# Optimization experiments

Measured on AMD Instinct MI355X. Metric: run time of the kernel, lower is better.

Reference implementation:

```python
import jax, jax.numpy as jnp
import numpy as np

INPUT_SIZE = 64
HIDDEN_SIZE = 256


def setup_inputs() -> dict:
    key = jax.random.key(0)
    ks = jax.random.split(key, 20)
    I, H = INPUT_SIZE, HIDDEN_SIZE
    s = 0.05
    inp = {
        "x": jax.random.normal(ks[0], (256, 512, I), jnp.float32),
        # LSTM params (PyTorch layout: [4H, in], gate order i,f,g,o)
        "w_ih": jax.random.normal(ks[1], (4 * H, I), jnp.float32) * s,
        "w_hh": jax.random.normal(ks[2], (4 * H, H), jnp.float32) * s,
        "b_ih": jax.random.normal(ks[3], (4 * H,), jnp.float32) * s,
        "b_hh": jax.random.normal(ks[4], (4 * H,), jnp.float32) * s,
        # fc_pit: H -> 64 -> 1
        "pit_w1": jax.random.normal(ks[5], (64, H), jnp.float32) * s,
        "pit_b1": jax.random.normal(ks[6], (64,), jnp.float32) * s,
        "pit_w2": jax.random.normal(ks[7], (1, 64), jnp.float32) * s,
        "pit_b2": jax.random.normal(ks[8], (1,), jnp.float32) * s,
        # fc_time: H+1 -> 64 -> 1
        "time_w1": jax.random.normal(ks[9], (64, H + 1), jnp.float32) * s,
        "time_b1": jax.random.normal(ks[10], (64,), jnp.float32) * s,
        "time_w2": jax.random.normal(ks[11], (1, 64), jnp.float32) * s,
        "time_b2": jax.random.normal(ks[12], (1,), jnp.float32) * s,
        "ar_w1": jax.random.normal(ks[13], (64, I + 2), jnp.float32) * s,
        "ar_b1": jax.random.normal(ks[14], (64,), jnp.float32) * s,
        "ar_w2": jax.random.normal(ks[15], (I, 64), jnp.float32) * s,
        "ar_b2": jax.random.normal(ks[16], (I,), jnp.float32) * s,
    }
    return inp


def _forward(x, w_ih, w_hh, b_ih, b_hh, pit_w1, pit_b1, pit_w2, pit_b2,
             time_w1, time_b1, time_w2, time_b2, ar_w1, ar_b1, ar_w2, ar_b2):
    B, S, I = x.shape
    H = w_hh.shape[1]

    def step(carry, x_orig_t):
        x_t, h, c = carry  # x_t: [B, I], h/c: [B, H]
        gates = x_t @ w_ih.T + b_ih + h @ w_hh.T + b_hh  # [B, 4H]
        i_g, f_g, g_g, o_g = jnp.split(gates, 4, axis=-1)
        i_g = jax.nn.sigmoid(i_g)
        f_g = jax.nn.sigmoid(f_g)
        g_g = jnp.tanh(g_g)
        o_g = jax.nn.sigmoid(o_g)
        c = f_g * c + i_g * g_g
        h = o_g * jnp.tanh(c)
        pit = jax.nn.relu(h @ pit_w1.T + pit_b1) @ pit_w2.T + pit_b2  # [B, 1]
        t_in = jnp.concatenate([h, pit], axis=1)  # [B, H+1]
        time = jax.nn.relu(t_in @ time_w1.T + time_b1) @ time_w2.T + time_b2  # [B, 1]
        ar_in = jnp.concatenate([pit, time, x_orig_t], axis=-1)  # [B, I+2]
        nxt = jax.nn.relu(ar_in @ ar_w1.T + ar_b1) @ ar_w2.T + ar_b2  # [B, I]
        return (nxt, h, c), (pit[:, 0], time[:, 0], nxt)

    h0 = jnp.zeros((B, H), x.dtype)
    c0 = jnp.zeros((B, H), x.dtype)
    x0 = x[:, 0, :]
    x_sbI = jnp.swapaxes(x, 0, 1)  # [S, B, I] original inputs fed at each step
    _, (pits, times, nxts) = jax.lax.scan(step, (x0, h0, c0), x_sbI)
    pit_pred = pits.T  # [B, S]
    time_pred = times.T  # [B, S]
    ar_out = jnp.concatenate([x[:, :1, :], jnp.swapaxes(nxts, 0, 1)[:, : S - 1, :]], axis=1)
    return pit_pred, time_pred, ar_out


def reference(x, w_ih, w_hh, b_ih, b_hh, pit_w1, pit_b1, pit_w2, pit_b2,
              time_w1, time_b1, time_w2, time_b2, ar_w1, ar_b1, ar_w2, ar_b2):
    return _forward(x, w_ih, w_hh, b_ih, b_hh, pit_w1, pit_b1, pit_w2, pit_b2,
                    time_w1, time_b1, time_w2, time_b2, ar_w1, ar_b1, ar_w2, ar_b2)
```

## Files before the change

### kernel.cpp

```cpp
#include <hip/hip_runtime.h>
#include <hip/hip_bf16.h>
#include <hip/hip_fp8.h>


typedef float f32x4 __attribute__((ext_vector_type(4)));
typedef short s16x8 __attribute__((ext_vector_type(8)));

#define S_LEN 512
#define I_DIM 64
#define NT    512

#define WSTRIDE8 45056
#define WSB_BF   360448
#define PREP_N   368640

#define OUT_PIT  0
#define OUT_TIME 131072
#define OUT_AR   262144

#define AF8 336
#define XLD 72

__device__ __forceinline__ float sigf(float x) {
  return 1.0f / (1.0f + __expf(-x));
}
__device__ __forceinline__ float tanh_fast(float x) {
  float c = fminf(fmaxf(x, -15.0f), 15.0f);
  float e = __expf(2.0f * c);
  return (e - 1.0f) / (e + 1.0f);
}
__device__ __forceinline__ unsigned short f2bf(float f) {
  __hip_bfloat16 h = __float2bfloat16(f);
  return *reinterpret_cast<unsigned short*>(&h);
}
__device__ __forceinline__ unsigned char f2f8(float v) {
  __hip_fp8_e4m3 q(v);
  return *reinterpret_cast<unsigned char*>(&q);
}
__device__ __forceinline__ void sync_lds() {
  asm volatile("s_waitcnt lgkmcnt(0)" ::: "memory");
  __builtin_amdgcn_s_barrier();
  asm volatile("" ::: "memory");
}
__device__ __forceinline__ void gld16(const void* g, void* l) {
  __builtin_amdgcn_global_load_lds(
      (const __attribute__((address_space(1))) unsigned int*)g,
      (__attribute__((address_space(3))) unsigned int*)l, 16, 0, 0);
}

__global__ void prep_kernel(const float* __restrict__ w_ih,
                            const float* __restrict__ w_hh,
                            const float* __restrict__ pit_w1,
                            const float* __restrict__ time_w1,
                            const float* __restrict__ ar_w1,
                            const float* __restrict__ ar_w2,
                            unsigned char* __restrict__ ws8) {
  int idx = blockIdx.x * 256 + threadIdx.x;
  if (idx >= PREP_N) return;
  if (idx < WSB_BF) {
    int w  = idx / WSTRIDE8;
    int p8 = idx - w * WSTRIDE8;
    int f  = p8 >> 9;
    int b  = p8 & 511;
    int lane = b >> 3, e = b & 7;
    int lrow = lane & 15, lgrp = lane >> 4;
    float v;
    if (f < 8) {
      int row = (w & 3) * 16 + lrow;
      int col = f * 32 + lgrp * 8 + e;
      v = (w < 4) ? pit_w1[row * 256 + col] : time_w1[row * 257 + col];
    } else {
      int g = f - 8;
      int ktidx = g >> 3, qm = g & 7;
      int kt = (ktidx < 8) ? ktidx + 2 : ktidx - 8;
      int row = (qm >> 1) * 256 + w * 32 + (qm & 1) * 16 + lrow;
      int col = kt * 32 + lgrp * 8 + e;
      v = (col < I_DIM) ? w_ih[row * I_DIM + col] : w_hh[row * 256 + col - I_DIM];
    }
    ws8[idx] = f2f8(v);
  } else {
    int e2 = idx - WSB_BF;
    int lane = (e2 >> 3) & 63;
    int e    = e2 & 7;
    int lrow = lane & 15, lgrp = lane >> 4;
    float v;
    if (e2 < 4096) {
      int f = e2 >> 9, wv = f >> 1, kt = f & 1;
      v = ar_w1[(wv * 16 + lrow) * 66 + 2 + kt * 32 + lgrp * 8 + e];
    } else {
      int f = (e2 - 4096) >> 9, wv = f >> 1, kt = f & 1;
      v = ar_w2[(wv * 16 + lrow) * 64 + kt * 32 + lgrp * 8 + e];
    }
    ((unsigned short*)(ws8 + WSB_BF))[e2] = f2bf(v);
  }
}

#define A8FRAG(kt) (*(const long*)&A_f8[lrow][(kt) * 32 + 8 * lgrp])

#define DMA4F(byteoff, slot)                                                   \
  do {                                                                         \
    const unsigned char* g_ = wg8l + (byteoff);                                \
    gld16(g_,        &stg8[wave][slot][0]);                                    \
    gld16(g_ + 1024, &stg8[wave][slot][1024]);                                 \
    gld16(g_ + 2048, &stg8[wave][slot][2048]);                                 \
    gld16(g_ + 3072, &stg8[wave][slot][3072]);                                 \
  } while (0)
#define DMA2F(byteoff, slot)                                                   \
  do {                                                                         \
    const unsigned char* g_ = wg8l + (byteoff);                                \
    gld16(g_,        &stg8[wave][slot][0]);                                    \
    gld16(g_ + 1024, &stg8[wave][slot][1024]);                                 \
  } while (0)

#define CHEADF(slot, N)                                                        \
  do {                                                                         \
    asm volatile("s_waitcnt vmcnt(" #N ")" ::: "memory");                      \
    _Pragma("unroll")                                                          \
    for (int k_ = 0; k_ < 8; ++k_) {                                           \
      long b_ = *(const long*)&stg8[wave][slot][k_ * 512 + lane * 8];          \
      hacc = __builtin_amdgcn_mfma_f32_16x16x32_fp8_fp8(hfr8[k_], b_,          \
                                                        hacc, 0, 0, 0);        \
    }                                                                          \
    asm volatile("s_waitcnt lgkmcnt(0)" ::: "memory");                         \
  } while (0)
#define GCHUNK8(af, slot, N)                                                   \
  do {                                                                         \
    asm volatile("s_waitcnt vmcnt(" #N ")" ::: "memory");                      \
    _Pragma("unroll")                                                          \
    for (int s_ = 0; s_ < 8; ++s_) {                                           \
      long b_ = *(const long*)&stg8[wave][slot][s_ * 512 + lane * 8];          \
      acc2[s_] = __builtin_amdgcn_mfma_f32_16x16x32_fp8_fp8(                   \
          (af), b_, acc2[s_], 0, 0, 0);                                        \
    }                                                                          \
    asm volatile("s_waitcnt lgkmcnt(0)" ::: "memory");                         \
  } while (0)
#define GHALF4(af, slot, N, qb)                                                \
  do {                                                                         \
    asm volatile("s_waitcnt vmcnt(" #N ")" ::: "memory");                      \
    _Pragma("unroll")                                                          \
    for (int s_ = 0; s_ < 4; ++s_) {                                           \
      long b_ = *(const long*)&stg8[wave][slot][s_ * 512 + lane * 8];          \
      acc2[(qb) + s_] = __builtin_amdgcn_mfma_f32_16x16x32_fp8_fp8(            \
          (af), b_, acc2[(qb) + s_], 0, 0, 0);                                 \
    }                                                                          \
    asm volatile("s_waitcnt lgkmcnt(0)" ::: "memory");                         \
  } while (0)

__global__ __launch_bounds__(NT, 2) void rnn_kernel(
    const float* __restrict__ x,
    const float* __restrict__ b_ih, const float* __restrict__ b_hh,
    const float* __restrict__ pit_b1, const float* __restrict__ pit_w2,
    const float* __restrict__ pit_b2,
    const float* __restrict__ time_w1, const float* __restrict__ time_b1,
    const float* __restrict__ time_w2, const float* __restrict__ time_b2,
    const float* __restrict__ ar_w1, const float* __restrict__ ar_b1,
    const float* __restrict__ ar_b2,
    const unsigned char* __restrict__ ws8,
    float* __restrict__ out)
{
  __shared__ __align__(16) unsigned char  A_f8[16][AF8];
  __shared__ __align__(16) unsigned short xo_lds[16][XLD];
  __shared__ __align__(16) unsigned short ar1_lds[16][XLD];
  __shared__ __align__(16) unsigned char  stg8[8][3][4096];
  __shared__ float pitp[4][16];
  __shared__ float timep[4][16];

  const int tid  = threadIdx.x;
  const int wave = tid >> 6;
  const int lane = tid & 63;
  const int lrow = lane & 15;
  const int lgrp = lane >> 4;
  const int b0   = blockIdx.x * 16;
  const int hcol = (wave & 3) * 16 + lrow;
  const unsigned char* wg8l = ws8 + wave * WSTRIDE8 + lane * 16;
  const unsigned char* wg8  = ws8 + wave * WSTRIDE8;
  const unsigned short* wsb = (const unsigned short*)(ws8 + WSB_BF);

  for (int i = tid; i < 16 * AF8; i += NT) (&A_f8[0][0])[i] = 0;

  float gbias[8];
#pragma unroll
  for (int qm = 0; qm < 8; ++qm) {
    int g = (qm >> 1) * 256 + wave * 32 + (qm & 1) * 16 + lrow;
    gbias[qm] = b_ih[g] + b_hh[g];
  }
  s16x8 arw[2];
  float pb1v = 0, pw2v = 0, tb1v = 0, tw2v = 0, twlv = 0;
  float ab1v = 0, arpv = 0, artv = 0, ab2v = 0;
  if (wave < 4) {
    arw[0] = *(const s16x8*)&wsb[((wave & 3) * 2 + 0) * 512 + lane * 8];
    arw[1] = *(const s16x8*)&wsb[((wave & 3) * 2 + 1) * 512 + lane * 8];
    pb1v = pit_b1[hcol]; pw2v = pit_w2[hcol];
    ab1v = ar_b1[hcol];  arpv = ar_w1[hcol * 66]; artv = ar_w1[hcol * 66 + 1];
  } else {
    arw[0] = *(const s16x8*)&wsb[4096 + ((wave & 3) * 2 + 0) * 512 + lane * 8];
    arw[1] = *(const s16x8*)&wsb[4096 + ((wave & 3) * 2 + 1) * 512 + lane * 8];
    tb1v = time_b1[hcol]; tw2v = time_w2[hcol];
    twlv = time_w1[hcol * 257 + 256]; ab2v = ar_b2[hcol];
  }
  const float pb2 = pit_b2[0], tb2 = time_b2[0];

  const int srow = tid >> 5;
  const int sc2  = (tid & 31) * 2;
  const size_t xbase = (size_t)(b0 + srow) * S_LEN * I_DIM + sc2;
  float2 xpre = *reinterpret_cast<const float2*>(&x[xbase]);
  __syncthreads();
  A_f8[srow][sc2]     = f2f8(xpre.x);
  A_f8[srow][sc2 + 1] = f2f8(xpre.y);
  *reinterpret_cast<float2*>(&out[OUT_AR + xbase]) = xpre;

  float cst[2][4];
#pragma unroll
  for (int m = 0; m < 2; ++m)
#pragma unroll
    for (int r = 0; r < 4; ++r) cst[m][r] = 0.0f;
  __syncthreads();

  f32x4 acc2[8];
#pragma unroll
  for (int qm = 0; qm < 8; ++qm) {
    f32x4 tv; tv[0] = tv[1] = tv[2] = tv[3] = gbias[qm];
    acc2[qm] = tv;
  }
  {
    long a0 = A8FRAG(0);
#pragma unroll
    for (int qm = 0; qm < 8; ++qm) {
      long b = *(const long*)(wg8 + 36864 + qm * 512 + lane * 8);
      acc2[qm] = __builtin_amdgcn_mfma_f32_16x16x32_fp8_fp8(a0, b, acc2[qm], 0, 0, 0);
    }
    long a1 = A8FRAG(1);
#pragma unroll
    for (int qm = 0; qm < 8; ++qm) {
      long b = *(const long*)(wg8 + 40960 + qm * 512 + lane * 8);
      acc2[qm] = __builtin_amdgcn_mfma_f32_16x16x32_fp8_fp8(a1, b, acc2[qm], 0, 0, 0);
    }
  }
  asm volatile("s_waitcnt vmcnt(0)" ::: "memory");
  DMA4F(0, 0);
  DMA4F(4096, 1);
  DMA4F(8192, 2);

  for (int t = 0; t < S_LEN; ++t) {
    xo_lds[srow][sc2]     = f2bf(xpre.x);
    xo_lds[srow][sc2 + 1] = f2bf(xpre.y);
    if (t + 1 < S_LEN)
      xpre = *reinterpret_cast<const float2*>(&x[xbase + (size_t)(t + 1) * I_DIM]);

#pragma unroll
    for (int m = 0; m < 2; ++m)
#pragma unroll
      for (int r = 0; r < 4; ++r) {
        float ig = sigf(acc2[0 + m][r]);
        float fg = sigf(acc2[2 + m][r]);
        float gg = tanh_fast(acc2[4 + m][r]);
        float og = sigf(acc2[6 + m][r]);
        float c  = fg * cst[m][r] + ig * gg;
        cst[m][r] = c;
        A_f8[lgrp * 4 + r][64 + wave * 32 + m * 16 + lrow] = f2f8(og * tanh_fast(c));
      }
#pragma unroll
    for (int qm = 0; qm < 8; ++qm) {
      f32x4 tv; tv[0] = tv[1] = tv[2] = tv[3] = gbias[qm];
      acc2[qm] = tv;
    }
    sync_lds();

    long hfr8[8];
#pragma unroll
    for (int k = 0; k < 8; ++k)
      hfr8[k] = *(const long*)&A_f8[lrow][64 + k * 32 + 8 * lgrp];

    f32x4 hacc;
    {
      float hb = (wave < 4) ? pb1v : tb1v;
      hacc[0] = hacc[1] = hacc[2] = hacc[3] = hb;
    }
    CHEADF(0, 8);            DMA4F(12288, 0);
    GCHUNK8(hfr8[0], 1, 8);  DMA4F(16384, 1);
    GCHUNK8(hfr8[1], 2, 8);  DMA4F(20480, 2);

    if (wave < 4) {
      float v[4];
#pragma unroll
      for (int r = 0; r < 4; ++r) v[r] = fmaxf(hacc[r], 0.0f) * pw2v;
#pragma unroll
      for (int off = 1; off < 16; off <<= 1)
#pragma unroll
        for (int r = 0; r < 4; ++r) v[r] += __shfl_xor(v[r], off);
      if (lrow == 0) {
#pragma unroll
        for (int r = 0; r < 4; ++r) pitp[wave][lgrp * 4 + r] = v[r];
      }
    }
    GCHUNK8(hfr8[2], 0, 8);  DMA4F(24576, 0);
    GCHUNK8(hfr8[3], 1, 8);  DMA4F(28672, 1);
    sync_lds();

    float pv[4];
#pragma unroll
    for (int r = 0; r < 4; ++r) {
      int row = lgrp * 4 + r;
      pv[r] = pitp[0][row] + pitp[1][row] + pitp[2][row] + pitp[3][row] + pb2;
    }
    f32x4 aracc;
    if (wave < 4) {
      aracc[0] = aracc[1] = aracc[2] = aracc[3] = ab1v;
#pragma unroll
      for (int kt = 0; kt < 2; ++kt) {
        s16x8 aX = *(const s16x8*)&xo_lds[lrow][kt * 32 + 8 * lgrp];
        aracc = __builtin_amdgcn_mfma_f32_16x16x32_bf16(aX, arw[kt], aracc, 0, 0, 0);
      }
      if (wave == 0 && lane < 16) {
        float pvs = pitp[0][lane] + pitp[1][lane] + pitp[2][lane] + pitp[3][lane] + pb2;
        out[OUT_PIT + (size_t)(b0 + lane) * S_LEN + t] = pvs;
      }
    } else {
      float v[4];
#pragma unroll
      for (int r = 0; r < 4; ++r)
        v[r] = fmaxf(hacc[r] + pv[r] * twlv, 0.0f) * tw2v;
#pragma unroll
      for (int off = 1; off < 16; off <<= 1)
#pragma unroll
        for (int r = 0; r < 4; ++r) v[r] += __shfl_xor(v[r], off);
      if (lrow == 0) {
#pragma unroll
        for (int r = 0; r < 4; ++r) timep[wave & 3][lgrp * 4 + r] = v[r];
      }
    }
    GCHUNK8(hfr8[4], 2, 8);  DMA4F(32768, 2);
    GCHUNK8(hfr8[5], 0, 8);  DMA4F(36864, 0);
    sync_lds();

    float tvv[4];
#pragma unroll
    for (int r = 0; r < 4; ++r) {
      int row = lgrp * 4 + r;
      tvv[r] = timep[0][row] + timep[1][row] + timep[2][row] + timep[3][row] + tb2;
    }
    if (wave < 4) {
#pragma unroll
      for (int r = 0; r < 4; ++r) {
        float a1 = aracc[r] + pv[r] * arpv + tvv[r] * artv;
        ar1_lds[lgrp * 4 + r][hcol] = f2bf(fmaxf(a1, 0.0f));
      }
    } else if (wave == 4 && lane < 16) {
      float tvs = timep[0][lane] + timep[1][lane] + timep[2][lane] + timep[3][lane] + tb2;
      out[OUT_TIME + (size_t)(b0 + lane) * S_LEN + t] = tvs;
    }
    GCHUNK8(hfr8[6], 1, 8);  DMA2F(40960, 1);
    GCHUNK8(hfr8[7], 2, 6);  DMA2F(43008, 2);
    sync_lds();

    if (wave >= 4) {
      f32x4 nacc;
      nacc[0] = nacc[1] = nacc[2] = nacc[3] = ab2v;
#pragma unroll
      for (int kt = 0; kt < 2; ++kt) {
        s16x8 aR = *(const s16x8*)&ar1_lds[lrow][kt * 32 + 8 * lgrp];
        nacc = __builtin_amdgcn_mfma_f32_16x16x32_bf16(aR, arw[kt], nacc, 0, 0, 0);
      }
#pragma unroll
      for (int r = 0; r < 4; ++r) {
        int row = lgrp * 4 + r;
        float nv = nacc[r];
        A_f8[row][hcol] = f2f8(nv);
        if (t < S_LEN - 1)
          out[OUT_AR + (size_t)(b0 + row) * S_LEN * I_DIM + (size_t)(t + 1) * I_DIM + hcol] = nv;
      }
    }
    sync_lds();

    {
      long a0 = A8FRAG(0);
      GCHUNK8(a0, 0, 4);     DMA4F(0, 0);
      long a1 = A8FRAG(1);
      GHALF4(a1, 1, 6, 0);   DMA4F(4096, 1);
      GHALF4(a1, 2, 8, 4);   DMA4F(8192, 2);
    }
  }
}

extern "C" void kernel_launch(void* const* d_in, const int* in_sizes, int n_in,
                              void* d_out, int out_size, void* d_ws, size_t ws_size,
                              hipStream_t stream) {
  const float* x       = (const float*)d_in[0];
  const float* w_ih    = (const float*)d_in[1];
  const float* w_hh    = (const float*)d_in[2];
  const float* b_ih    = (const float*)d_in[3];
  const float* b_hh    = (const float*)d_in[4];
  const float* pit_w1  = (const float*)d_in[5];
  const float* pit_b1  = (const float*)d_in[6];
  const float* pit_w2  = (const float*)d_in[7];
  const float* pit_b2  = (const float*)d_in[8];
  const float* time_w1 = (const float*)d_in[9];
  const float* time_b1 = (const float*)d_in[10];
  const float* time_w2 = (const float*)d_in[11];
  const float* time_b2 = (const float*)d_in[12];
  const float* ar_w1   = (const float*)d_in[13];
  const float* ar_b1   = (const float*)d_in[14];
  const float* ar_w2   = (const float*)d_in[15];
  const float* ar_b2   = (const float*)d_in[16];
  unsigned char* ws8   = (unsigned char*)d_ws;
  float* out           = (float*)d_out;

  prep_kernel<<<dim3((PREP_N + 255) / 256), dim3(256), 0, stream>>>(
      w_ih, w_hh, pit_w1, time_w1, ar_w1, ar_w2, ws8);
  rnn_kernel<<<dim3(16), dim3(NT), 0, stream>>>(
      x, b_ih, b_hh, pit_b1, pit_w2, pit_b2,
      time_w1, time_b1, time_w2, time_b2,
      ar_w1, ar_b1, ar_b2, ws8, out);
}
```

Before: 3.796 ms.

## Keep pit/time head FP8 weights resident in LDS instead of streaming per step

The pit_w1 and time_w1 FP8 fragments are moved out of each wave's streamed weight block into a separate workspace region. Every block loads them once into 32 KB of LDS, and each step reads them from there. The per-wave streamed weight chunk shrinks, and the DMA/GCHUNK schedule is reshuffled to match the new offsets and vmcnt counts. The goal is less global/L2 traffic per timestep, paid for with higher LDS usage, which may reduce occupancy from the launch bound of 2 blocks per CU.

```diff
diff --git a/kernel.cpp b/kernel.cpp
--- a/kernel.cpp
+++ b/kernel.cpp
@@ -10,7 +10,9 @@
 #define I_DIM 64
 #define NT    512
 
-#define WSTRIDE8 45056
+#define WSTRIDE8 40960
+#define WSB_P8   327680
+#define WSB_T8   344064
 #define WSB_BF   360448
 #define PREP_N   368640
 
@@ -57,27 +59,34 @@
                             unsigned char* __restrict__ ws8) {
   int idx = blockIdx.x * 256 + threadIdx.x;
   if (idx >= PREP_N) return;
-  if (idx < WSB_BF) {
+  if (idx < WSB_P8) {
     int w  = idx / WSTRIDE8;
     int p8 = idx - w * WSTRIDE8;
     int f  = p8 >> 9;
     int b  = p8 & 511;
     int lane = b >> 3, e = b & 7;
     int lrow = lane & 15, lgrp = lane >> 4;
-    float v;
-    if (f < 8) {
-      int row = (w & 3) * 16 + lrow;
-      int col = f * 32 + lgrp * 8 + e;
-      v = (w < 4) ? pit_w1[row * 256 + col] : time_w1[row * 257 + col];
-    } else {
-      int g = f - 8;
-      int ktidx = g >> 3, qm = g & 7;
-      int kt = (ktidx < 8) ? ktidx + 2 : ktidx - 8;
-      int row = (qm >> 1) * 256 + w * 32 + (qm & 1) * 16 + lrow;
-      int col = kt * 32 + lgrp * 8 + e;
-      v = (col < I_DIM) ? w_ih[row * I_DIM + col] : w_hh[row * 256 + col - I_DIM];
-    }
+    int ktidx = f >> 3, qm = f & 7;
+    int kt = (ktidx < 8) ? ktidx + 2 : ktidx - 8;
+    int row = (qm >> 1) * 256 + w * 32 + (qm & 1) * 16 + lrow;
+    int col = kt * 32 + lgrp * 8 + e;
+    float v = (col < I_DIM) ? w_ih[row * I_DIM + col]
+                            : w_hh[row * 256 + col - I_DIM];
     ws8[idx] = f2f8(v);
+  } else if (idx < WSB_T8) {
+    int p = idx - WSB_P8;
+    int f = p >> 9, b = p & 511;
+    int wv = f >> 3, kt = f & 7;
+    int lane = b >> 3, e = b & 7;
+    int lrow = lane & 15, lgrp = lane >> 4;
+    ws8[idx] = f2f8(pit_w1[(wv * 16 + lrow) * 256 + kt * 32 + lgrp * 8 + e]);
+  } else if (idx < WSB_BF) {
+    int p = idx - WSB_T8;
+    int f = p >> 9, b = p & 511;
+    int wv = f >> 3, kt = f & 7;
+    int lane = b >> 3, e = b & 7;
+    int lrow = lane & 15, lgrp = lane >> 4;
+    ws8[idx] = f2f8(time_w1[(wv * 16 + lrow) * 257 + kt * 32 + lgrp * 8 + e]);
   } else {
     int e2 = idx - WSB_BF;
     int lane = (e2 >> 3) & 63;
@@ -112,17 +121,6 @@
     gld16(g_ + 1024, &stg8[wave][slot][1024]);                                 \
   } while (0)
 
-#define CHEADF(slot, N)                                                        \
-  do {                                                                         \
-    asm volatile("s_waitcnt vmcnt(" #N ")" ::: "memory");                      \
-    _Pragma("unroll")                                                          \
-    for (int k_ = 0; k_ < 8; ++k_) {                                           \
-      long b_ = *(const long*)&stg8[wave][slot][k_ * 512 + lane * 8];          \
-      hacc = __builtin_amdgcn_mfma_f32_16x16x32_fp8_fp8(hfr8[k_], b_,          \
-                                                        hacc, 0, 0, 0);        \
-    }                                                                          \
-    asm volatile("s_waitcnt lgkmcnt(0)" ::: "memory");                         \
-  } while (0)
 #define GCHUNK8(af, slot, N)                                                   \
   do {                                                                         \
     asm volatile("s_waitcnt vmcnt(" #N ")" ::: "memory");                      \
@@ -161,6 +159,8 @@
   __shared__ __align__(16) unsigned char  A_f8[16][AF8];
   __shared__ __align__(16) unsigned short xo_lds[16][XLD];
   __shared__ __align__(16) unsigned short ar1_lds[16][XLD];
+  __shared__ __align__(16) unsigned char  pit8_lds[16384];
+  __shared__ __align__(16) unsigned char  tim8_lds[16384];
   __shared__ __align__(16) unsigned char  stg8[8][3][4096];
   __shared__ float pitp[4][16];
   __shared__ float timep[4][16];
@@ -176,6 +176,10 @@
   const unsigned char* wg8  = ws8 + wave * WSTRIDE8;
   const unsigned short* wsb = (const unsigned short*)(ws8 + WSB_BF);
 
+  for (int c = tid; c < 2048; c += NT) {
+    *(long*)&pit8_lds[c * 8] = *(const long*)&ws8[WSB_P8 + c * 8];
+    *(long*)&tim8_lds[c * 8] = *(const long*)&ws8[WSB_T8 + c * 8];
+  }
   for (int i = tid; i < 16 * AF8; i += NT) (&A_f8[0][0])[i] = 0;
 
   float gbias[8];
@@ -226,13 +230,13 @@
     long a0 = A8FRAG(0);
 #pragma unroll
     for (int qm = 0; qm < 8; ++qm) {
-      long b = *(const long*)(wg8 + 36864 + qm * 512 + lane * 8);
+      long b = *(const long*)(wg8 + (64 + qm) * 512 + lane * 8);
       acc2[qm] = __builtin_amdgcn_mfma_f32_16x16x32_fp8_fp8(a0, b, acc2[qm], 0, 0, 0);
     }
     long a1 = A8FRAG(1);
 #pragma unroll
     for (int qm = 0; qm < 8; ++qm) {
-      long b = *(const long*)(wg8 + 40960 + qm * 512 + lane * 8);
+      long b = *(const long*)(wg8 + (72 + qm) * 512 + lane * 8);
       acc2[qm] = __builtin_amdgcn_mfma_f32_16x16x32_fp8_fp8(a1, b, acc2[qm], 0, 0, 0);
     }
   }
@@ -275,11 +279,13 @@
     {
       float hb = (wave < 4) ? pb1v : tb1v;
       hacc[0] = hacc[1] = hacc[2] = hacc[3] = hb;
-    }
-    CHEADF(0, 8);            DMA4F(12288, 0);
-    GCHUNK8(hfr8[0], 1, 8);  DMA4F(16384, 1);
-    GCHUNK8(hfr8[1], 2, 8);  DMA4F(20480, 2);
-
+      const unsigned char* hbp = (wave < 4) ? pit8_lds : tim8_lds;
+#pragma unroll
+      for (int kt = 0; kt < 8; ++kt) {
+        long bH = *(const long*)&hbp[((wave & 3) * 8 + kt) * 512 + lane * 8];
+        hacc = __builtin_amdgcn_mfma_f32_16x16x32_fp8_fp8(hfr8[kt], bH, hacc, 0, 0, 0);
+      }
+    }
     if (wave < 4) {
       float v[4];
 #pragma unroll
@@ -293,8 +299,10 @@
         for (int r = 0; r < 4; ++r) pitp[wave][lgrp * 4 + r] = v[r];
       }
     }
-    GCHUNK8(hfr8[2], 0, 8);  DMA4F(24576, 0);
-    GCHUNK8(hfr8[3], 1, 8);  DMA4F(28672, 1);
+    GCHUNK8(hfr8[0], 0, 8); DMA4F(12288, 0);
+    GCHUNK8(hfr8[1], 1, 8); DMA4F(16384, 1);
+    GCHUNK8(hfr8[2], 2, 8); DMA4F(20480, 2);
+    GCHUNK8(hfr8[3], 0, 8); DMA4F(24576, 0);
     sync_lds();
 
     float pv[4];
@@ -329,8 +337,8 @@
         for (int r = 0; r < 4; ++r) timep[wave & 3][lgrp * 4 + r] = v[r];
       }
     }
-    GCHUNK8(hfr8[4], 2, 8);  DMA4F(32768, 2);
-    GCHUNK8(hfr8[5], 0, 8);  DMA4F(36864, 0);
+    GCHUNK8(hfr8[4], 1, 8); DMA4F(28672, 1);
+    GCHUNK8(hfr8[5], 2, 8); DMA2F(32768, 2);
     sync_lds();
 
     float tvv[4];
@@ -349,8 +357,8 @@
       float tvs = timep[0][lane] + timep[1][lane] + timep[2][lane] + timep[3][lane] + tb2;
       out[OUT_TIME + (size_t)(b0 + lane) * S_LEN + t] = tvs;
     }
-    GCHUNK8(hfr8[6], 1, 8);  DMA2F(40960, 1);
-    GCHUNK8(hfr8[7], 2, 6);  DMA2F(43008, 2);
+    GCHUNK8(hfr8[6], 0, 6); DMA2F(34816, 0);
+    GCHUNK8(hfr8[7], 1, 4); DMA2F(36864, 1);
     sync_lds();
 
     if (wave >= 4) {
@@ -374,10 +382,11 @@
 
     {
       long a0 = A8FRAG(0);
-      GCHUNK8(a0, 0, 4);     DMA4F(0, 0);
+      GHALF4(a0, 2, 4, 0); DMA2F(38912, 2);
+      GHALF4(a0, 0, 4, 4); DMA4F(0, 0);
       long a1 = A8FRAG(1);
-      GHALF4(a1, 1, 6, 0);   DMA4F(4096, 1);
-      GHALF4(a1, 2, 8, 4);   DMA4F(8192, 2);
+      GHALF4(a1, 1, 6, 0); DMA4F(4096, 1);
+      GHALF4(a1, 2, 8, 4); DMA4F(8192, 2);
     }
   }
 }
```

Result: faster. 3.429 ms (-9.7%).
